# Kernel optimization log

Measured on AMD Instinct MI355X. Metric: run time of the kernel, lower is better.

Reference implementation:

```python
import jax, jax.numpy as jnp
import numpy as np

N_NODES = 50000
N_EDGES = 800000
D = 128
BATCHSIZE = 64


def setup_inputs() -> dict:
    key = jax.random.key(0)
    k1, k2, k3, k4 = jax.random.split(key, 4)
    x = jax.random.normal(k1, (N_NODES, D), dtype=jnp.float32)
    eps = jnp.zeros((1,), dtype=jnp.float32)
    W_pred = jax.random.normal(k2, (D, D), dtype=jnp.float32) * (1.0 / np.sqrt(D))
    b_pred = jnp.zeros((D,), dtype=jnp.float32)
    edge_index = jax.random.randint(k3, (2, N_EDGES), 0, N_NODES, dtype=jnp.int64)
    batch = jnp.sort(jax.random.randint(k4, (N_NODES,), 0, BATCHSIZE, dtype=jnp.int64))
    return {"x": x, "eps": eps, "W_pred": W_pred, "b_pred": b_pred,
            "edge_index": edge_index, "batch": batch}


def reference(x, eps, W_pred, b_pred, edge_index, batch):
    src, dst = edge_index[0], edge_index[1]
    # spmm: sum of neighbor features for each destination node [N, D]
    agg = jax.ops.segment_sum(x[src], dst, num_segments=N_NODES)
    # eps-weighted self update (apply_func=None, norm=None)
    out = (1.0 + eps) * x + agg
    out = jax.nn.relu(out)  # activation='relu'
    # linear_prediction then per-graph scatter-add pooling
    pooled = out @ W_pred + b_pred  # [N, pooled_features]
    pooled2 = jax.ops.segment_sum(pooled, batch, num_segments=BATCHSIZE)  # [B, pooled]
    return out, pooled2
```

## Files before the change

kernel.cpp:

```cpp
#include <hip/hip_runtime.h>
#include <hip/hip_bf16.h>

#define N_NODES 50000
#define N_EDGES 800000
#define D 128
#define BATCHSIZE 64

#define CHUNK_BITS 7
#define CHUNK 128
#define NBUCKETS 391
#define NBUCKETS_PAD 392
#define CAP 2400
#define GS_PAD 16

#define FB_TILE 2048
#define NTILES ((N_EDGES + FB_TILE - 1) / FB_TILE)
#define FB_THREADS 256
#define FB_GRID NTILES
#define EPT 8

__device__ inline unsigned f2bf(float f) {
    union { float f; unsigned u; } c; c.f = f;
    unsigned u = c.u;
    return (u + 0x7fffu + ((u >> 16) & 1u)) >> 16;
}

__device__ inline float4 bf4_to_f4(uint2 u) {
    union { unsigned u; float f; } a, b, c, d;
    a.u = u.x << 16; b.u = u.x & 0xffff0000u;
    c.u = u.y << 16; d.u = u.y & 0xffff0000u;
    float4 r; r.x = a.f; r.y = b.f; r.z = c.f; r.w = d.f;
    return r;
}

__global__ __launch_bounds__(FB_THREADS) void bin_convert_kernel(
    const float* __restrict__ x,
    unsigned short* __restrict__ xb,
    const int* __restrict__ edge_index,
    int* __restrict__ gcur,
    int* __restrict__ bucket,
    float* __restrict__ pooled2,
    int gs)
{
    __shared__ int hist[NBUCKETS_PAD];
    __shared__ int gbase[NBUCKETS_PAD];

    int t = threadIdx.x;
    int blk = blockIdx.x;

    for (int i = blk * FB_THREADS + t; i < BATCHSIZE * D; i += FB_GRID * FB_THREADS)
        pooled2[i] = 0.0f;

    if (xb != nullptr) {
        const int TOT8 = N_NODES * D / 8;
        for (int i = blk * FB_THREADS + t; i < TOT8; i += FB_GRID * FB_THREADS) {
            float4 v0 = *(const float4*)(x + (size_t)i * 8);
            float4 v1 = *(const float4*)(x + (size_t)i * 8 + 4);
            uint4 pk;
            pk.x = f2bf(v0.x) | (f2bf(v0.y) << 16);
            pk.y = f2bf(v0.z) | (f2bf(v0.w) << 16);
            pk.z = f2bf(v1.x) | (f2bf(v1.y) << 16);
            pk.w = f2bf(v1.z) | (f2bf(v1.w) << 16);
            *(uint4*)(xb + (size_t)i * 8) = pk;
        }
    }

    for (int i = t; i < NBUCKETS_PAD; i += FB_THREADS) hist[i] = 0;
    __syncthreads();

    int base = blk * FB_TILE;
    int lim = N_EDGES - base; if (lim > FB_TILE) lim = FB_TILE;

    int bkt[EPT];
    int pack[EPT];
#pragma unroll
    for (int j = 0; j < EPT / 4; ++j) {
        int e4 = (j * FB_THREADS + t) * 4;
#pragma unroll
        for (int k = 0; k < 4; ++k) bkt[j * 4 + k] = -1;
        if (e4 < lim) {
            int4 s4 = *(const int4*)(edge_index + base + e4);
            int4 d4 = *(const int4*)(edge_index + N_EDGES + base + e4);
            int ss[4] = { s4.x, s4.y, s4.z, s4.w };
            int dd[4] = { d4.x, d4.y, d4.z, d4.w };
#pragma unroll
            for (int k = 0; k < 4; ++k) {
                int b = dd[k] >> CHUNK_BITS;
                bkt[j * 4 + k] = b;
                pack[j * 4 + k] = (ss[k] << CHUNK_BITS) | (dd[k] & (CHUNK - 1));
                atomicAdd(&hist[b], 1);
            }
        }
    }
    __syncthreads();

    for (int i = t; i < NBUCKETS; i += FB_THREADS) {
        int c = hist[i];
        gbase[i] = c ? atomicAdd(&gcur[i * gs], c) : 0;
        hist[i] = 0;
    }
    __syncthreads();

#pragma unroll
    for (int k = 0; k < EPT; ++k) {
        int b = bkt[k];
        if (b >= 0) {
            int pos = gbase[b] + atomicAdd(&hist[b], 1);
            if (pos < CAP) bucket[(size_t)b * CAP + pos] = pack[k];
        }
    }
}

template<bool BF16>
__global__ __launch_bounds__(1024) void gather_kernel(
    const float* __restrict__ x,
    const unsigned short* __restrict__ xb,
    const float* __restrict__ eps,
    const int* __restrict__ batch,
    const int* __restrict__ gcur,
    const int* __restrict__ bucket,
    const float* __restrict__ W,
    const float* __restrict__ b_pred,
    float* __restrict__ out,
    float* __restrict__ pooled2,
    int gs)
{
    __shared__ int   ebuf[CAP];
    __shared__ int   sorted[CAP];
    __shared__ int   hist[CHUNK];
    __shared__ int   offs[CHUNK + 1];
    __shared__ int   cursor[CHUNK];
    __shared__ float pool[8 * D];
    __shared__ int   pcount[8];

    int c = blockIdx.x;
    int t = threadIdx.x;
    int lane = t & 31;
    int g = t >> 5;

    if (t < CHUNK) hist[t] = 0;
    if (t < 8) pcount[t] = 0;
    for (int i = t; i < 8 * D; i += 1024) pool[i] = 0.0f;
    int cnt = gcur[(size_t)c * gs];
    if (cnt > CAP) cnt = CAP;
    __syncthreads();

    for (int i = t; i < cnt; i += 1024) {
        int p = bucket[(size_t)c * CAP + i];
        ebuf[i] = p;
        atomicAdd(&hist[p & (CHUNK - 1)], 1);
    }
    __syncthreads();

    if (t < 64) {
        int h0 = hist[2 * t], h1 = hist[2 * t + 1];
        int tot = h0 + h1;
        int incl = tot;
#pragma unroll
        for (int o = 1; o < 64; o <<= 1) {
            int y = __shfl_up(incl, o, 64);
            if (t >= o) incl += y;
        }
        int excl = incl - tot;
        offs[2 * t] = excl;          cursor[2 * t] = excl;
        offs[2 * t + 1] = excl + h0; cursor[2 * t + 1] = excl + h0;
        if (t == 63) offs[CHUNK] = incl;
    }
    __syncthreads();

    for (int i = t; i < cnt; i += 1024) {
        int p = ebuf[i];
        int pos = atomicAdd(&cursor[p & (CHUNK - 1)], 1);
        sorted[pos] = p >> CHUNK_BITS;
    }
    __syncthreads();

    int node0 = c << CHUNK_BITS;
    int base_b = batch[node0];
    float scale = 1.0f + eps[0];
    int dv_cur = -1;
    float4 ps = make_float4(0.f, 0.f, 0.f, 0.f);

#pragma unroll
    for (int k = 0; k < 4; ++k) {
        int d = 4 * g + k;
        int node = node0 + d;
        if (node >= N_NODES) break;
        int start = offs[d], end = offs[d + 1];
        float4 acc = make_float4(0.f, 0.f, 0.f, 0.f);
        int i = start;
        if (BF16) {
            for (; i + 4 <= end; i += 4) {
                int s0 = sorted[i], s1 = sorted[i + 1];
                int s2 = sorted[i + 2], s3 = sorted[i + 3];
                uint2 u0 = *(const uint2*)(xb + (size_t)s0 * D + lane * 4);
                uint2 u1 = *(const uint2*)(xb + (size_t)s1 * D + lane * 4);
                uint2 u2 = *(const uint2*)(xb + (size_t)s2 * D + lane * 4);
                uint2 u3 = *(const uint2*)(xb + (size_t)s3 * D + lane * 4);
                float4 v0 = bf4_to_f4(u0), v1 = bf4_to_f4(u1);
                float4 v2 = bf4_to_f4(u2), v3 = bf4_to_f4(u3);
                acc.x += (v0.x + v1.x) + (v2.x + v3.x);
                acc.y += (v0.y + v1.y) + (v2.y + v3.y);
                acc.z += (v0.z + v1.z) + (v2.z + v3.z);
                acc.w += (v0.w + v1.w) + (v2.w + v3.w);
            }
            for (; i < end; ++i) {
                uint2 u0 = *(const uint2*)(xb + (size_t)sorted[i] * D + lane * 4);
                float4 v0 = bf4_to_f4(u0);
                acc.x += v0.x; acc.y += v0.y; acc.z += v0.z; acc.w += v0.w;
            }
        } else {
            for (; i + 4 <= end; i += 4) {
                int s0 = sorted[i], s1 = sorted[i + 1];
                int s2 = sorted[i + 2], s3 = sorted[i + 3];
                const float4 v0 = *(const float4*)(x + (size_t)s0 * D + lane * 4);
                const float4 v1 = *(const float4*)(x + (size_t)s1 * D + lane * 4);
                const float4 v2 = *(const float4*)(x + (size_t)s2 * D + lane * 4);
                const float4 v3 = *(const float4*)(x + (size_t)s3 * D + lane * 4);
                acc.x += (v0.x + v1.x) + (v2.x + v3.x);
                acc.y += (v0.y + v1.y) + (v2.y + v3.y);
                acc.z += (v0.z + v1.z) + (v2.z + v3.z);
                acc.w += (v0.w + v1.w) + (v2.w + v3.w);
            }
            for (; i < end; ++i) {
                const float4 v0 = *(const float4*)(x + (size_t)sorted[i] * D + lane * 4);
                acc.x += v0.x; acc.y += v0.y; acc.z += v0.z; acc.w += v0.w;
            }
        }
        const float4 xv = *(const float4*)(x + (size_t)node * D + lane * 4);
        float4 o;
        o.x = fmaxf(fmaf(scale, xv.x, acc.x), 0.0f);
        o.y = fmaxf(fmaf(scale, xv.y, acc.y), 0.0f);
        o.z = fmaxf(fmaf(scale, xv.z, acc.z), 0.0f);
        o.w = fmaxf(fmaf(scale, xv.w, acc.w), 0.0f);
        *(float4*)(out + (size_t)node * D + lane * 4) = o;

        int dv = batch[node] - base_b;
        if (dv < 8) {
            if (dv != dv_cur) {
                if (dv_cur >= 0) {
                    float* pp = &pool[dv_cur * D + lane * 4];
                    atomicAdd(pp + 0, ps.x); atomicAdd(pp + 1, ps.y);
                    atomicAdd(pp + 2, ps.z); atomicAdd(pp + 3, ps.w);
                }
                ps = make_float4(0.f, 0.f, 0.f, 0.f);
                dv_cur = dv;
            }
            ps.x += o.x; ps.y += o.y; ps.z += o.z; ps.w += o.w;
            if (lane == 0) atomicAdd(&pcount[dv], 1);
        }
    }
    if (dv_cur >= 0) {
        float* pp = &pool[dv_cur * D + lane * 4];
        atomicAdd(pp + 0, ps.x); atomicAdd(pp + 1, ps.y);
        atomicAdd(pp + 2, ps.z); atomicAdd(pp + 3, ps.w);
    }
    __syncthreads();

    int lastnode = node0 + CHUNK - 1;
    if (lastnode >= N_NODES) lastnode = N_NODES - 1;
    int used = batch[lastnode] - base_b + 1;
    if (used > 8) used = 8;
    if (t < D) {
        for (int dv = 0; dv < used; ++dv) {
            float acc = (float)pcount[dv] * b_pred[t];
            const float* prow = &pool[dv * D];
#pragma unroll 8
            for (int k = 0; k < D; ++k) {
                acc = fmaf(prow[k], W[(size_t)k * D + t], acc);
            }
            atomicAdd(&pooled2[(size_t)(base_b + dv) * D + t], acc);
        }
    }
}


__global__ void edge_scatter_kernel(const float* __restrict__ x,
                                    const int* __restrict__ edge_index,
                                    float* __restrict__ agg) {
    int tid = blockIdx.x * blockDim.x + threadIdx.x;
    int lane = tid & 31;
    int e = tid >> 5;
    if (e >= N_EDGES) return;
    int src = edge_index[e];
    int dst = edge_index[N_EDGES + e];
    const float4 v = *(const float4*)(x + (size_t)src * D + lane * 4);
    float* dp = agg + (size_t)dst * D + lane * 4;
    atomicAdd(dp + 0, v.x);
    atomicAdd(dp + 1, v.y);
    atomicAdd(dp + 2, v.z);
    atomicAdd(dp + 3, v.w);
}

__global__ void finalize_kernel(const float* __restrict__ x,
                                const float* __restrict__ eps,
                                const int* __restrict__ batch,
                                float* __restrict__ out,
                                float* __restrict__ Sf,
                                float* __restrict__ counts) {
    int tid = blockIdx.x * blockDim.x + threadIdx.x;
    int lane = tid & 31;
    int node = tid >> 5;
    if (node >= N_NODES) return;
    float scale = 1.0f + eps[0];
    const float4 xv = *(const float4*)(x + (size_t)node * D + lane * 4);
    float4 av = *(float4*)(out + (size_t)node * D + lane * 4);
    float4 o;
    o.x = fmaxf(fmaf(scale, xv.x, av.x), 0.0f);
    o.y = fmaxf(fmaf(scale, xv.y, av.y), 0.0f);
    o.z = fmaxf(fmaf(scale, xv.z, av.z), 0.0f);
    o.w = fmaxf(fmaf(scale, xv.w, av.w), 0.0f);
    *(float4*)(out + (size_t)node * D + lane * 4) = o;
    int b = batch[node];
    float* sp = Sf + (size_t)b * D + lane * 4;
    atomicAdd(sp + 0, o.x);
    atomicAdd(sp + 1, o.y);
    atomicAdd(sp + 2, o.z);
    atomicAdd(sp + 3, o.w);
    if (lane == 0) atomicAdd(counts + b, 1.0f);
}

__global__ void pool_gemm_fallback_kernel(const float* __restrict__ Sf,
                                          const float* __restrict__ counts,
                                          const float* __restrict__ W,
                                          const float* __restrict__ b_pred,
                                          float* __restrict__ pooled2) {
    int b = blockIdx.x;
    int j = threadIdx.x;
    float acc = counts[b] * b_pred[j];
    const float* srow = Sf + (size_t)b * D;
#pragma unroll 8
    for (int k = 0; k < D; ++k) {
        acc = fmaf(srow[k], W[(size_t)k * D + j], acc);
    }
    pooled2[(size_t)b * D + j] = acc;
}

extern "C" void kernel_launch(void* const* d_in, const int* in_sizes, int n_in,
                              void* d_out, int out_size, void* d_ws, size_t ws_size,
                              hipStream_t stream) {
    const float* x      = (const float*)d_in[0];
    const float* eps    = (const float*)d_in[1];
    const float* W_pred = (const float*)d_in[2];
    const float* b_pred = (const float*)d_in[3];
    const int*   eidx   = (const int*)d_in[4];
    const int*   batch  = (const int*)d_in[5];

    float* out     = (float*)d_out;
    float* pooled2 = (float*)d_out + (size_t)N_NODES * D;

    const size_t xb_ints = (size_t)N_NODES * D / 2;
    const size_t buck    = (size_t)NBUCKETS * CAP;

    const size_t need_pad_full  = ((size_t)NBUCKETS_PAD * GS_PAD + buck + xb_ints) * 4;
    const size_t need_full      = ((size_t)NBUCKETS_PAD + buck + xb_ints) * 4;
    const size_t need_pad_mid   = ((size_t)NBUCKETS_PAD * GS_PAD + buck) * 4;
    const size_t need_mid       = ((size_t)NBUCKETS_PAD + buck) * 4;

    if (ws_size >= need_mid) {
        int gs = (ws_size >= (ws_size >= need_full ? need_pad_full : need_pad_mid))
                     ? GS_PAD : 1;
        size_t gcur_ints = (size_t)NBUCKETS_PAD * gs;
        int* gcur   = (int*)d_ws;
        int* bucket = (int*)d_ws + gcur_ints;
        bool full = (ws_size >= (gs == GS_PAD ? need_pad_full : need_full));
        unsigned short* xb = full
            ? (unsigned short*)((int*)d_ws + gcur_ints + buck) : nullptr;

        hipMemsetAsync(gcur, 0, gcur_ints * 4, stream);

        bin_convert_kernel<<<FB_GRID, FB_THREADS, 0, stream>>>(
            x, xb, eidx, gcur, bucket, pooled2, gs);
        if (full) {
            gather_kernel<true><<<NBUCKETS, 1024, 0, stream>>>(
                x, xb, eps, batch, gcur, bucket, W_pred, b_pred, out, pooled2, gs);
        } else {
            gather_kernel<false><<<NBUCKETS, 1024, 0, stream>>>(
                x, (const unsigned short*)nullptr, eps, batch, gcur, bucket,
                W_pred, b_pred, out, pooled2, gs);
        }
    } else {
        float* Sf      = (float*)d_ws;
        float* countsf = (float*)d_ws + BATCHSIZE * D;
        hipMemsetAsync(out, 0, (size_t)N_NODES * D * sizeof(float), stream);
        hipMemsetAsync(d_ws, 0, (BATCHSIZE * D + BATCHSIZE) * sizeof(float), stream);
        {
            long long total = (long long)N_EDGES * 32;
            int blocks = (int)((total + 255) / 256);
            edge_scatter_kernel<<<blocks, 256, 0, stream>>>(x, eidx, out);
        }
        {
            long long total = (long long)N_NODES * 32;
            int blocks = (int)((total + 255) / 256);
            finalize_kernel<<<blocks, 256, 0, stream>>>(x, eps, batch, out, Sf, countsf);
        }
        pool_gemm_fallback_kernel<<<BATCHSIZE, D, 0, stream>>>(Sf, countsf, W_pred, b_pred, pooled2);
    }
}
```

Baseline: 145.8 us.

## Fuse binning and gather into one cooperative kernel with grid sync

Merges the edge-binning/bf16-conversion kernel and the per-chunk gather kernel into a single cooperative launch of 391 blocks × 512 threads, separated by a grid-wide barrier. Shared buffers are reused for the binning histogram. Each warp group now processes 8 destination nodes instead of 4. This removes a kernel launch boundary but halves per-block threads in the gather phase and adds grid-sync cost.

```diff
diff --git a/kernel.cpp b/kernel.cpp
--- a/kernel.cpp
+++ b/kernel.cpp
@@ -1,5 +1,8 @@
 #include <hip/hip_runtime.h>
 #include <hip/hip_bf16.h>
+#include <hip/hip_cooperative_groups.h>
+
+namespace cg = cooperative_groups;
 
 #define N_NODES 50000
 #define N_EDGES 800000
@@ -13,11 +16,8 @@
 #define CAP 2400
 #define GS_PAD 16
 
+#define FT 512
 #define FB_TILE 2048
-#define NTILES ((N_EDGES + FB_TILE - 1) / FB_TILE)
-#define FB_THREADS 256
-#define FB_GRID NTILES
-#define EPT 8
 
 __device__ inline unsigned f2bf(float f) {
     union { float f; unsigned u; } c; c.f = f;
@@ -33,92 +33,15 @@
     return r;
 }
 
-__global__ __launch_bounds__(FB_THREADS) void bin_convert_kernel(
+template<bool BF16>
+__global__ __launch_bounds__(FT) void fused_kernel(
     const float* __restrict__ x,
     unsigned short* __restrict__ xb,
-    const int* __restrict__ edge_index,
+    const int* __restrict__ eidx,
     int* __restrict__ gcur,
     int* __restrict__ bucket,
-    float* __restrict__ pooled2,
-    int gs)
-{
-    __shared__ int hist[NBUCKETS_PAD];
-    __shared__ int gbase[NBUCKETS_PAD];
-
-    int t = threadIdx.x;
-    int blk = blockIdx.x;
-
-    for (int i = blk * FB_THREADS + t; i < BATCHSIZE * D; i += FB_GRID * FB_THREADS)
-        pooled2[i] = 0.0f;
-
-    if (xb != nullptr) {
-        const int TOT8 = N_NODES * D / 8;
-        for (int i = blk * FB_THREADS + t; i < TOT8; i += FB_GRID * FB_THREADS) {
-            float4 v0 = *(const float4*)(x + (size_t)i * 8);
-            float4 v1 = *(const float4*)(x + (size_t)i * 8 + 4);
-            uint4 pk;
-            pk.x = f2bf(v0.x) | (f2bf(v0.y) << 16);
-            pk.y = f2bf(v0.z) | (f2bf(v0.w) << 16);
-            pk.z = f2bf(v1.x) | (f2bf(v1.y) << 16);
-            pk.w = f2bf(v1.z) | (f2bf(v1.w) << 16);
-            *(uint4*)(xb + (size_t)i * 8) = pk;
-        }
-    }
-
-    for (int i = t; i < NBUCKETS_PAD; i += FB_THREADS) hist[i] = 0;
-    __syncthreads();
-
-    int base = blk * FB_TILE;
-    int lim = N_EDGES - base; if (lim > FB_TILE) lim = FB_TILE;
-
-    int bkt[EPT];
-    int pack[EPT];
-#pragma unroll
-    for (int j = 0; j < EPT / 4; ++j) {
-        int e4 = (j * FB_THREADS + t) * 4;
-#pragma unroll
-        for (int k = 0; k < 4; ++k) bkt[j * 4 + k] = -1;
-        if (e4 < lim) {
-            int4 s4 = *(const int4*)(edge_index + base + e4);
-            int4 d4 = *(const int4*)(edge_index + N_EDGES + base + e4);
-            int ss[4] = { s4.x, s4.y, s4.z, s4.w };
-            int dd[4] = { d4.x, d4.y, d4.z, d4.w };
-#pragma unroll
-            for (int k = 0; k < 4; ++k) {
-                int b = dd[k] >> CHUNK_BITS;
-                bkt[j * 4 + k] = b;
-                pack[j * 4 + k] = (ss[k] << CHUNK_BITS) | (dd[k] & (CHUNK - 1));
-                atomicAdd(&hist[b], 1);
-            }
-        }
-    }
-    __syncthreads();
-
-    for (int i = t; i < NBUCKETS; i += FB_THREADS) {
-        int c = hist[i];
-        gbase[i] = c ? atomicAdd(&gcur[i * gs], c) : 0;
-        hist[i] = 0;
-    }
-    __syncthreads();
-
-#pragma unroll
-    for (int k = 0; k < EPT; ++k) {
-        int b = bkt[k];
-        if (b >= 0) {
-            int pos = gbase[b] + atomicAdd(&hist[b], 1);
-            if (pos < CAP) bucket[(size_t)b * CAP + pos] = pack[k];
-        }
-    }
-}
-
-template<bool BF16>
-__global__ __launch_bounds__(1024) void gather_kernel(
-    const float* __restrict__ x,
-    const unsigned short* __restrict__ xb,
     const float* __restrict__ eps,
     const int* __restrict__ batch,
-    const int* __restrict__ gcur,
-    const int* __restrict__ bucket,
     const float* __restrict__ W,
     const float* __restrict__ b_pred,
     float* __restrict__ out,
@@ -133,19 +56,88 @@
     __shared__ float pool[8 * D];
     __shared__ int   pcount[8];
 
-    int c = blockIdx.x;
     int t = threadIdx.x;
+    int blk = blockIdx.x;
+    const int GSTRIDE = NBUCKETS * FT;
+
+    int* histA  = ebuf;
+    int* gbaseA = sorted;
+
+    for (int i = blk * FT + t; i < BATCHSIZE * D; i += GSTRIDE)
+        pooled2[i] = 0.0f;
+
+    if (BF16) {
+        const int TOT8 = N_NODES * D / 8;
+        for (int i = blk * FT + t; i < TOT8; i += GSTRIDE) {
+            float4 v0 = *(const float4*)(x + (size_t)i * 8);
+            float4 v1 = *(const float4*)(x + (size_t)i * 8 + 4);
+            uint4 pk;
+            pk.x = f2bf(v0.x) | (f2bf(v0.y) << 16);
+            pk.y = f2bf(v0.z) | (f2bf(v0.w) << 16);
+            pk.z = f2bf(v1.x) | (f2bf(v1.y) << 16);
+            pk.w = f2bf(v1.z) | (f2bf(v1.w) << 16);
+            *(uint4*)(xb + (size_t)i * 8) = pk;
+        }
+    }
+
+    for (int i = t; i < NBUCKETS_PAD; i += FT) histA[i] = 0;
+    __syncthreads();
+
+    int base = blk * FB_TILE;
+    int lim = N_EDGES - base; if (lim > FB_TILE) lim = FB_TILE;
+
+    int bkt[4];
+    int pack[4];
+    {
+        int e4 = t * 4;
+#pragma unroll
+        for (int k = 0; k < 4; ++k) bkt[k] = -1;
+        if (e4 < lim) {
+            int4 s4 = *(const int4*)(eidx + base + e4);
+            int4 d4 = *(const int4*)(eidx + N_EDGES + base + e4);
+            int ss[4] = { s4.x, s4.y, s4.z, s4.w };
+            int dd[4] = { d4.x, d4.y, d4.z, d4.w };
+#pragma unroll
+            for (int k = 0; k < 4; ++k) {
+                int b = dd[k] >> CHUNK_BITS;
+                bkt[k] = b;
+                pack[k] = (ss[k] << CHUNK_BITS) | (dd[k] & (CHUNK - 1));
+                atomicAdd(&histA[b], 1);
+            }
+        }
+    }
+    __syncthreads();
+
+    for (int i = t; i < NBUCKETS; i += FT) {
+        int cc = histA[i];
+        gbaseA[i] = cc ? atomicAdd(&gcur[(size_t)i * gs], cc) : 0;
+        histA[i] = 0;
+    }
+    __syncthreads();
+
+#pragma unroll
+    for (int k = 0; k < 4; ++k) {
+        int b = bkt[k];
+        if (b >= 0) {
+            int pos = gbaseA[b] + atomicAdd(&histA[b], 1);
+            if (pos < CAP) bucket[(size_t)b * CAP + pos] = pack[k];
+        }
+    }
+
+    cg::this_grid().sync();
+
+    int c = blk;
     int lane = t & 31;
     int g = t >> 5;
 
     if (t < CHUNK) hist[t] = 0;
     if (t < 8) pcount[t] = 0;
-    for (int i = t; i < 8 * D; i += 1024) pool[i] = 0.0f;
+    for (int i = t; i < 8 * D; i += FT) pool[i] = 0.0f;
     int cnt = gcur[(size_t)c * gs];
     if (cnt > CAP) cnt = CAP;
     __syncthreads();
 
-    for (int i = t; i < cnt; i += 1024) {
+    for (int i = t; i < cnt; i += FT) {
         int p = bucket[(size_t)c * CAP + i];
         ebuf[i] = p;
         atomicAdd(&hist[p & (CHUNK - 1)], 1);
@@ -168,7 +160,7 @@
     }
     __syncthreads();
 
-    for (int i = t; i < cnt; i += 1024) {
+    for (int i = t; i < cnt; i += FT) {
         int p = ebuf[i];
         int pos = atomicAdd(&cursor[p & (CHUNK - 1)], 1);
         sorted[pos] = p >> CHUNK_BITS;
@@ -182,8 +174,8 @@
     float4 ps = make_float4(0.f, 0.f, 0.f, 0.f);
 
 #pragma unroll
-    for (int k = 0; k < 4; ++k) {
-        int d = 4 * g + k;
+    for (int k = 0; k < 8; ++k) {
+        int d = 8 * g + k;
         int node = node0 + d;
         if (node >= N_NODES) break;
         int start = offs[d], end = offs[d + 1];
@@ -369,15 +361,23 @@
 
         hipMemsetAsync(gcur, 0, gcur_ints * 4, stream);
 
-        bin_convert_kernel<<<FB_GRID, FB_THREADS, 0, stream>>>(
-            x, xb, eidx, gcur, bucket, pooled2, gs);
         if (full) {
-            gather_kernel<true><<<NBUCKETS, 1024, 0, stream>>>(
-                x, xb, eps, batch, gcur, bucket, W_pred, b_pred, out, pooled2, gs);
+            auto kfun = fused_kernel<true>;
+            void* args[] = { (void*)&x, (void*)&xb, (void*)&eidx, (void*)&gcur,
+                             (void*)&bucket, (void*)&eps, (void*)&batch,
+                             (void*)&W_pred, (void*)&b_pred, (void*)&out,
+                             (void*)&pooled2, (void*)&gs };
+            hipLaunchCooperativeKernel(reinterpret_cast<void*>(kfun),
+                                       dim3(NBUCKETS), dim3(FT), args, 0, stream);
         } else {
-            gather_kernel<false><<<NBUCKETS, 1024, 0, stream>>>(
-                x, (const unsigned short*)nullptr, eps, batch, gcur, bucket,
-                W_pred, b_pred, out, pooled2, gs);
+            unsigned short* xb_null = nullptr;
+            auto kfun = fused_kernel<false>;
+            void* args[] = { (void*)&x, (void*)&xb_null, (void*)&eidx, (void*)&gcur,
+                             (void*)&bucket, (void*)&eps, (void*)&batch,
+                             (void*)&W_pred, (void*)&b_pred, (void*)&out,
+                             (void*)&pooled2, (void*)&gs };
+            hipLaunchCooperativeKernel(reinterpret_cast<void*>(kfun),
+                                       dim3(NBUCKETS), dim3(FT), args, 0, stream);
         }
     } else {
         float* Sf      = (float*)d_ws;
```

Measured after the change: 231.5 us. 58.8% more time.

## Slice gather by source-node range so all warps sweep x in lockstep

Applied to the files above, without the earlier changes.

Sorts each chunk's edges by (source slice, destination) with a 512-bin histogram and shared-memory scan. The gather loop then runs over four source-node slices, keeping per-node accumulators in registers, so all warps in a block touch the same region of x at the same time for better L2/cache locality. Launch bounds are also raised to request two blocks per CU. In exchange it adds a multi-barrier Hillis-Steele scan, more shared memory and more registers, and each warp's work is split into more, shorter loops.

```diff
diff --git a/kernel.cpp b/kernel.cpp
--- a/kernel.cpp
+++ b/kernel.cpp
@@ -12,6 +12,10 @@
 #define NBUCKETS_PAD 392
 #define CAP 2400
 #define GS_PAD 16
+
+#define NSLICE 4
+#define SLICE_DIV 12500
+#define NBINS (NSLICE * CHUNK)
 
 #define FB_TILE 2048
 #define NTILES ((N_EDGES + FB_TILE - 1) / FB_TILE)
@@ -112,7 +116,7 @@
 }
 
 template<bool BF16>
-__global__ __launch_bounds__(1024) void gather_kernel(
+__global__ __launch_bounds__(1024, 2) void gather_kernel(
     const float* __restrict__ x,
     const unsigned short* __restrict__ xb,
     const float* __restrict__ eps,
@@ -127,9 +131,9 @@
 {
     __shared__ int   ebuf[CAP];
     __shared__ int   sorted[CAP];
-    __shared__ int   hist[CHUNK];
-    __shared__ int   offs[CHUNK + 1];
-    __shared__ int   cursor[CHUNK];
+    __shared__ int   hist[NBINS];
+    __shared__ int   offs[NBINS + 1];
+    __shared__ int   cursor[NBINS];
     __shared__ float pool[8 * D];
     __shared__ int   pcount[8];
 
@@ -138,7 +142,7 @@
     int lane = t & 31;
     int g = t >> 5;
 
-    if (t < CHUNK) hist[t] = 0;
+    for (int i = t; i < NBINS; i += 1024) hist[i] = 0;
     if (t < 8) pcount[t] = 0;
     for (int i = t; i < 8 * D; i += 1024) pool[i] = 0.0f;
     int cnt = gcur[(size_t)c * gs];
@@ -148,29 +152,30 @@
     for (int i = t; i < cnt; i += 1024) {
         int p = bucket[(size_t)c * CAP + i];
         ebuf[i] = p;
-        atomicAdd(&hist[p & (CHUNK - 1)], 1);
-    }
-    __syncthreads();
-
-    if (t < 64) {
-        int h0 = hist[2 * t], h1 = hist[2 * t + 1];
-        int tot = h0 + h1;
-        int incl = tot;
-#pragma unroll
-        for (int o = 1; o < 64; o <<= 1) {
-            int y = __shfl_up(incl, o, 64);
-            if (t >= o) incl += y;
-        }
-        int excl = incl - tot;
-        offs[2 * t] = excl;          cursor[2 * t] = excl;
-        offs[2 * t + 1] = excl + h0; cursor[2 * t + 1] = excl + h0;
-        if (t == 63) offs[CHUNK] = incl;
-    }
+        int key = (int)((unsigned)(p >> CHUNK_BITS) / SLICE_DIV) * CHUNK + (p & (CHUNK - 1));
+        atomicAdd(&hist[key], 1);
+    }
+    __syncthreads();
+
+    if (t < NBINS) cursor[t] = hist[t];
+    __syncthreads();
+    for (int st = 1; st < NBINS; st <<= 1) {
+        int v = 0;
+        if (t < NBINS && t >= st) v = cursor[t - st];
+        __syncthreads();
+        if (t < NBINS) cursor[t] += v;
+        __syncthreads();
+    }
+    if (t < NBINS) offs[t + 1] = cursor[t];
+    if (t == 0) offs[0] = 0;
+    __syncthreads();
+    if (t < NBINS) cursor[t] = offs[t];
     __syncthreads();
 
     for (int i = t; i < cnt; i += 1024) {
         int p = ebuf[i];
-        int pos = atomicAdd(&cursor[p & (CHUNK - 1)], 1);
+        int key = (int)((unsigned)(p >> CHUNK_BITS) / SLICE_DIV) * CHUNK + (p & (CHUNK - 1));
+        int pos = atomicAdd(&cursor[key], 1);
         sorted[pos] = p >> CHUNK_BITS;
     }
     __syncthreads();
@@ -178,61 +183,71 @@
     int node0 = c << CHUNK_BITS;
     int base_b = batch[node0];
     float scale = 1.0f + eps[0];
+
+    float4 acc[4];
+#pragma unroll
+    for (int k = 0; k < 4; ++k) acc[k] = make_float4(0.f, 0.f, 0.f, 0.f);
+
+    for (int s = 0; s < NSLICE; ++s) {
+#pragma unroll
+        for (int k = 0; k < 4; ++k) {
+            int d = 4 * g + k;
+            int i = offs[s * CHUNK + d], end = offs[s * CHUNK + d + 1];
+            float4 a = acc[k];
+            if (BF16) {
+                for (; i + 4 <= end; i += 4) {
+                    int s0 = sorted[i], s1 = sorted[i + 1];
+                    int s2 = sorted[i + 2], s3 = sorted[i + 3];
+                    uint2 u0 = *(const uint2*)(xb + (size_t)s0 * D + lane * 4);
+                    uint2 u1 = *(const uint2*)(xb + (size_t)s1 * D + lane * 4);
+                    uint2 u2 = *(const uint2*)(xb + (size_t)s2 * D + lane * 4);
+                    uint2 u3 = *(const uint2*)(xb + (size_t)s3 * D + lane * 4);
+                    float4 v0 = bf4_to_f4(u0), v1 = bf4_to_f4(u1);
+                    float4 v2 = bf4_to_f4(u2), v3 = bf4_to_f4(u3);
+                    a.x += (v0.x + v1.x) + (v2.x + v3.x);
+                    a.y += (v0.y + v1.y) + (v2.y + v3.y);
+                    a.z += (v0.z + v1.z) + (v2.z + v3.z);
+                    a.w += (v0.w + v1.w) + (v2.w + v3.w);
+                }
+                for (; i < end; ++i) {
+                    uint2 u0 = *(const uint2*)(xb + (size_t)sorted[i] * D + lane * 4);
+                    float4 v0 = bf4_to_f4(u0);
+                    a.x += v0.x; a.y += v0.y; a.z += v0.z; a.w += v0.w;
+                }
+            } else {
+                for (; i + 4 <= end; i += 4) {
+                    int s0 = sorted[i], s1 = sorted[i + 1];
+                    int s2 = sorted[i + 2], s3 = sorted[i + 3];
+                    const float4 v0 = *(const float4*)(x + (size_t)s0 * D + lane * 4);
+                    const float4 v1 = *(const float4*)(x + (size_t)s1 * D + lane * 4);
+                    const float4 v2 = *(const float4*)(x + (size_t)s2 * D + lane * 4);
+                    const float4 v3 = *(const float4*)(x + (size_t)s3 * D + lane * 4);
+                    a.x += (v0.x + v1.x) + (v2.x + v3.x);
+                    a.y += (v0.y + v1.y) + (v2.y + v3.y);
+                    a.z += (v0.z + v1.z) + (v2.z + v3.z);
+                    a.w += (v0.w + v1.w) + (v2.w + v3.w);
+                }
+                for (; i < end; ++i) {
+                    const float4 v0 = *(const float4*)(x + (size_t)sorted[i] * D + lane * 4);
+                    a.x += v0.x; a.y += v0.y; a.z += v0.z; a.w += v0.w;
+                }
+            }
+            acc[k] = a;
+        }
+    }
+
     int dv_cur = -1;
     float4 ps = make_float4(0.f, 0.f, 0.f, 0.f);
-
 #pragma unroll
     for (int k = 0; k < 4; ++k) {
-        int d = 4 * g + k;
-        int node = node0 + d;
+        int node = node0 + 4 * g + k;
         if (node >= N_NODES) break;
-        int start = offs[d], end = offs[d + 1];
-        float4 acc = make_float4(0.f, 0.f, 0.f, 0.f);
-        int i = start;
-        if (BF16) {
-            for (; i + 4 <= end; i += 4) {
-                int s0 = sorted[i], s1 = sorted[i + 1];
-                int s2 = sorted[i + 2], s3 = sorted[i + 3];
-                uint2 u0 = *(const uint2*)(xb + (size_t)s0 * D + lane * 4);
-                uint2 u1 = *(const uint2*)(xb + (size_t)s1 * D + lane * 4);
-                uint2 u2 = *(const uint2*)(xb + (size_t)s2 * D + lane * 4);
-                uint2 u3 = *(const uint2*)(xb + (size_t)s3 * D + lane * 4);
-                float4 v0 = bf4_to_f4(u0), v1 = bf4_to_f4(u1);
-                float4 v2 = bf4_to_f4(u2), v3 = bf4_to_f4(u3);
-                acc.x += (v0.x + v1.x) + (v2.x + v3.x);
-                acc.y += (v0.y + v1.y) + (v2.y + v3.y);
-                acc.z += (v0.z + v1.z) + (v2.z + v3.z);
-                acc.w += (v0.w + v1.w) + (v2.w + v3.w);
-            }
-            for (; i < end; ++i) {
-                uint2 u0 = *(const uint2*)(xb + (size_t)sorted[i] * D + lane * 4);
-                float4 v0 = bf4_to_f4(u0);
-                acc.x += v0.x; acc.y += v0.y; acc.z += v0.z; acc.w += v0.w;
-            }
-        } else {
-            for (; i + 4 <= end; i += 4) {
-                int s0 = sorted[i], s1 = sorted[i + 1];
-                int s2 = sorted[i + 2], s3 = sorted[i + 3];
-                const float4 v0 = *(const float4*)(x + (size_t)s0 * D + lane * 4);
-                const float4 v1 = *(const float4*)(x + (size_t)s1 * D + lane * 4);
-                const float4 v2 = *(const float4*)(x + (size_t)s2 * D + lane * 4);
-                const float4 v3 = *(const float4*)(x + (size_t)s3 * D + lane * 4);
-                acc.x += (v0.x + v1.x) + (v2.x + v3.x);
-                acc.y += (v0.y + v1.y) + (v2.y + v3.y);
-                acc.z += (v0.z + v1.z) + (v2.z + v3.z);
-                acc.w += (v0.w + v1.w) + (v2.w + v3.w);
-            }
-            for (; i < end; ++i) {
-                const float4 v0 = *(const float4*)(x + (size_t)sorted[i] * D + lane * 4);
-                acc.x += v0.x; acc.y += v0.y; acc.z += v0.z; acc.w += v0.w;
-            }
-        }
         const float4 xv = *(const float4*)(x + (size_t)node * D + lane * 4);
         float4 o;
-        o.x = fmaxf(fmaf(scale, xv.x, acc.x), 0.0f);
-        o.y = fmaxf(fmaf(scale, xv.y, acc.y), 0.0f);
-        o.z = fmaxf(fmaf(scale, xv.z, acc.z), 0.0f);
-        o.w = fmaxf(fmaf(scale, xv.w, acc.w), 0.0f);
+        o.x = fmaxf(fmaf(scale, xv.x, acc[k].x), 0.0f);
+        o.y = fmaxf(fmaf(scale, xv.y, acc[k].y), 0.0f);
+        o.z = fmaxf(fmaf(scale, xv.z, acc[k].z), 0.0f);
+        o.w = fmaxf(fmaf(scale, xv.w, acc[k].w), 0.0f);
         *(float4*)(out + (size_t)node * D + lane * 4) = o;
 
         int dv = batch[node] - base_b;
@@ -263,13 +278,13 @@
     if (used > 8) used = 8;
     if (t < D) {
         for (int dv = 0; dv < used; ++dv) {
-            float acc = (float)pcount[dv] * b_pred[t];
+            float acc2 = (float)pcount[dv] * b_pred[t];
             const float* prow = &pool[dv * D];
 #pragma unroll 8
             for (int k = 0; k < D; ++k) {
-                acc = fmaf(prow[k], W[(size_t)k * D + t], acc);
+                acc2 = fmaf(prow[k], W[(size_t)k * D + t], acc2);
             }
-            atomicAdd(&pooled2[(size_t)(base_b + dv) * D + t], acc);
+            atomicAdd(&pooled2[(size_t)(base_b + dv) * D + t], acc2);
         }
     }
 }
```

Measured after the change: 145.7 us, median of 2. Within noise of the previous version (-0.1%).

## Replace chunk bucketing and in-block sort with per-node fixed-capacity adjacency slots

Applied to the files above, without the earlier changes.

Edge binning now writes each source index straight into a fixed per-destination slot array (48 slots per node) using a global atomic counter per node. This removes the per-chunk bucket histogram, prefix scan and shared-memory counting sort in the gather kernel, which now just loads its 128 nodes' slot lists into shared memory. The cost is 800k scattered global atomics on 50k counters in place of block-local atomics, and silent truncation of any node with more than 48 in-edges. Launch bounds now request two 1024-thread blocks per CU.

```diff
diff --git a/kernel.cpp b/kernel.cpp
--- a/kernel.cpp
+++ b/kernel.cpp
@@ -9,15 +9,11 @@
 #define CHUNK_BITS 7
 #define CHUNK 128
 #define NBUCKETS 391
-#define NBUCKETS_PAD 392
-#define CAP 2400
-#define GS_PAD 16
-
-#define FB_TILE 2048
-#define NTILES ((N_EDGES + FB_TILE - 1) / FB_TILE)
+#define NNODE_PAD 50048
+#define SEG_CAP 48
+
 #define FB_THREADS 256
-#define FB_GRID NTILES
-#define EPT 8
+#define FB_GRID 391
 
 __device__ inline unsigned f2bf(float f) {
     union { float f; unsigned u; } c; c.f = f;
@@ -33,27 +29,25 @@
     return r;
 }
 
-__global__ __launch_bounds__(FB_THREADS) void bin_convert_kernel(
+__global__ __launch_bounds__(FB_THREADS) void csr_bin_convert(
     const float* __restrict__ x,
     unsigned short* __restrict__ xb,
     const int* __restrict__ edge_index,
-    int* __restrict__ gcur,
-    int* __restrict__ bucket,
-    float* __restrict__ pooled2,
-    int gs)
+    int* __restrict__ cnt,
+    int* __restrict__ seg,
+    float* __restrict__ pooled2)
 {
-    __shared__ int hist[NBUCKETS_PAD];
-    __shared__ int gbase[NBUCKETS_PAD];
-
     int t = threadIdx.x;
     int blk = blockIdx.x;
-
-    for (int i = blk * FB_THREADS + t; i < BATCHSIZE * D; i += FB_GRID * FB_THREADS)
+    int gid = blk * FB_THREADS + t;
+    const int gsz = FB_GRID * FB_THREADS;
+
+    for (int i = gid; i < BATCHSIZE * D; i += gsz)
         pooled2[i] = 0.0f;
 
     if (xb != nullptr) {
         const int TOT8 = N_NODES * D / 8;
-        for (int i = blk * FB_THREADS + t; i < TOT8; i += FB_GRID * FB_THREADS) {
+        for (int i = gid; i < TOT8; i += gsz) {
             float4 v0 = *(const float4*)(x + (size_t)i * 8);
             float4 v1 = *(const float4*)(x + (size_t)i * 8 + 4);
             uint4 pk;
@@ -65,71 +59,35 @@
         }
     }
 
-    for (int i = t; i < NBUCKETS_PAD; i += FB_THREADS) hist[i] = 0;
-    __syncthreads();
-
-    int base = blk * FB_TILE;
-    int lim = N_EDGES - base; if (lim > FB_TILE) lim = FB_TILE;
-
-    int bkt[EPT];
-    int pack[EPT];
+    const int TOTE4 = N_EDGES / 4;
+    for (int q = gid; q < TOTE4; q += gsz) {
+        int4 s4 = ((const int4*)edge_index)[q];
+        int4 d4 = ((const int4*)(edge_index + N_EDGES))[q];
+        int ss[4] = { s4.x, s4.y, s4.z, s4.w };
+        int dd[4] = { d4.x, d4.y, d4.z, d4.w };
 #pragma unroll
-    for (int j = 0; j < EPT / 4; ++j) {
-        int e4 = (j * FB_THREADS + t) * 4;
-#pragma unroll
-        for (int k = 0; k < 4; ++k) bkt[j * 4 + k] = -1;
-        if (e4 < lim) {
-            int4 s4 = *(const int4*)(edge_index + base + e4);
-            int4 d4 = *(const int4*)(edge_index + N_EDGES + base + e4);
-            int ss[4] = { s4.x, s4.y, s4.z, s4.w };
-            int dd[4] = { d4.x, d4.y, d4.z, d4.w };
-#pragma unroll
-            for (int k = 0; k < 4; ++k) {
-                int b = dd[k] >> CHUNK_BITS;
-                bkt[j * 4 + k] = b;
-                pack[j * 4 + k] = (ss[k] << CHUNK_BITS) | (dd[k] & (CHUNK - 1));
-                atomicAdd(&hist[b], 1);
-            }
-        }
-    }
-    __syncthreads();
-
-    for (int i = t; i < NBUCKETS; i += FB_THREADS) {
-        int c = hist[i];
-        gbase[i] = c ? atomicAdd(&gcur[i * gs], c) : 0;
-        hist[i] = 0;
-    }
-    __syncthreads();
-
-#pragma unroll
-    for (int k = 0; k < EPT; ++k) {
-        int b = bkt[k];
-        if (b >= 0) {
-            int pos = gbase[b] + atomicAdd(&hist[b], 1);
-            if (pos < CAP) bucket[(size_t)b * CAP + pos] = pack[k];
+        for (int k = 0; k < 4; ++k) {
+            int pos = atomicAdd(&cnt[dd[k]], 1);
+            if (pos < SEG_CAP) seg[(size_t)dd[k] * SEG_CAP + pos] = ss[k];
         }
     }
 }
 
 template<bool BF16>
-__global__ __launch_bounds__(1024) void gather_kernel(
+__global__ __launch_bounds__(1024, 2) void gather_csr(
     const float* __restrict__ x,
     const unsigned short* __restrict__ xb,
     const float* __restrict__ eps,
     const int* __restrict__ batch,
-    const int* __restrict__ gcur,
-    const int* __restrict__ bucket,
+    const int* __restrict__ cnt,
+    const int* __restrict__ seg,
     const float* __restrict__ W,
     const float* __restrict__ b_pred,
     float* __restrict__ out,
-    float* __restrict__ pooled2,
-    int gs)
+    float* __restrict__ pooled2)
 {
-    __shared__ int   ebuf[CAP];
-    __shared__ int   sorted[CAP];
-    __shared__ int   hist[CHUNK];
-    __shared__ int   offs[CHUNK + 1];
-    __shared__ int   cursor[CHUNK];
+    __shared__ int   segL[CHUNK * SEG_CAP];
+    __shared__ int   cntL[CHUNK];
     __shared__ float pool[8 * D];
     __shared__ int   pcount[8];
 
@@ -137,46 +95,23 @@
     int t = threadIdx.x;
     int lane = t & 31;
     int g = t >> 5;
-
-    if (t < CHUNK) hist[t] = 0;
+    int node0 = c << CHUNK_BITS;
+
+    if (t < CHUNK) {
+        int n = node0 + t;
+        int cc = (n < N_NODES) ? cnt[n] : 0;
+        cntL[t] = cc > SEG_CAP ? SEG_CAP : cc;
+    }
     if (t < 8) pcount[t] = 0;
     for (int i = t; i < 8 * D; i += 1024) pool[i] = 0.0f;
-    int cnt = gcur[(size_t)c * gs];
-    if (cnt > CAP) cnt = CAP;
+
+    for (int i = t; i < CHUNK * SEG_CAP; i += 1024) {
+        int n = node0 + i / SEG_CAP;
+        segL[i] = (n < N_NODES) ? seg[(size_t)node0 * SEG_CAP + i] : 0;
+    }
     __syncthreads();
 
-    for (int i = t; i < cnt; i += 1024) {
-        int p = bucket[(size_t)c * CAP + i];
-        ebuf[i] = p;
-        atomicAdd(&hist[p & (CHUNK - 1)], 1);
-    }
-    __syncthreads();
-
-    if (t < 64) {
-        int h0 = hist[2 * t], h1 = hist[2 * t + 1];
-        int tot = h0 + h1;
-        int incl = tot;
-#pragma unroll
-        for (int o = 1; o < 64; o <<= 1) {
-            int y = __shfl_up(incl, o, 64);
-            if (t >= o) incl += y;
-        }
-        int excl = incl - tot;
-        offs[2 * t] = excl;          cursor[2 * t] = excl;
-        offs[2 * t + 1] = excl + h0; cursor[2 * t + 1] = excl + h0;
-        if (t == 63) offs[CHUNK] = incl;
-    }
-    __syncthreads();
-
-    for (int i = t; i < cnt; i += 1024) {
-        int p = ebuf[i];
-        int pos = atomicAdd(&cursor[p & (CHUNK - 1)], 1);
-        sorted[pos] = p >> CHUNK_BITS;
-    }
-    __syncthreads();
-
-    int node0 = c << CHUNK_BITS;
-    int base_b = batch[node0];
+    int base_b = batch[node0 < N_NODES ? node0 : N_NODES - 1];
     float scale = 1.0f + eps[0];
     int dv_cur = -1;
     float4 ps = make_float4(0.f, 0.f, 0.f, 0.f);
@@ -186,13 +121,14 @@
         int d = 4 * g + k;
         int node = node0 + d;
         if (node >= N_NODES) break;
-        int start = offs[d], end = offs[d + 1];
+        const int* sp = &segL[d * SEG_CAP];
+        int end = cntL[d];
         float4 acc = make_float4(0.f, 0.f, 0.f, 0.f);
-        int i = start;
+        int i = 0;
         if (BF16) {
             for (; i + 4 <= end; i += 4) {
-                int s0 = sorted[i], s1 = sorted[i + 1];
-                int s2 = sorted[i + 2], s3 = sorted[i + 3];
+                int s0 = sp[i], s1 = sp[i + 1];
+                int s2 = sp[i + 2], s3 = sp[i + 3];
                 uint2 u0 = *(const uint2*)(xb + (size_t)s0 * D + lane * 4);
                 uint2 u1 = *(const uint2*)(xb + (size_t)s1 * D + lane * 4);
                 uint2 u2 = *(const uint2*)(xb + (size_t)s2 * D + lane * 4);
@@ -205,14 +141,14 @@
                 acc.w += (v0.w + v1.w) + (v2.w + v3.w);
             }
             for (; i < end; ++i) {
-                uint2 u0 = *(const uint2*)(xb + (size_t)sorted[i] * D + lane * 4);
+                uint2 u0 = *(const uint2*)(xb + (size_t)sp[i] * D + lane * 4);
                 float4 v0 = bf4_to_f4(u0);
                 acc.x += v0.x; acc.y += v0.y; acc.z += v0.z; acc.w += v0.w;
             }
         } else {
             for (; i + 4 <= end; i += 4) {
-                int s0 = sorted[i], s1 = sorted[i + 1];
-                int s2 = sorted[i + 2], s3 = sorted[i + 3];
+                int s0 = sp[i], s1 = sp[i + 1];
+                int s2 = sp[i + 2], s3 = sp[i + 3];
                 const float4 v0 = *(const float4*)(x + (size_t)s0 * D + lane * 4);
                 const float4 v1 = *(const float4*)(x + (size_t)s1 * D + lane * 4);
                 const float4 v2 = *(const float4*)(x + (size_t)s2 * D + lane * 4);
@@ -223,7 +159,7 @@
                 acc.w += (v0.w + v1.w) + (v2.w + v3.w);
             }
             for (; i < end; ++i) {
-                const float4 v0 = *(const float4*)(x + (size_t)sorted[i] * D + lane * 4);
+                const float4 v0 = *(const float4*)(x + (size_t)sp[i] * D + lane * 4);
                 acc.x += v0.x; acc.y += v0.y; acc.z += v0.z; acc.w += v0.w;
             }
         }
@@ -263,13 +199,13 @@
     if (used > 8) used = 8;
     if (t < D) {
         for (int dv = 0; dv < used; ++dv) {
-            float acc = (float)pcount[dv] * b_pred[t];
+            float acc2 = (float)pcount[dv] * b_pred[t];
             const float* prow = &pool[dv * D];
 #pragma unroll 8
             for (int k = 0; k < D; ++k) {
-                acc = fmaf(prow[k], W[(size_t)k * D + t], acc);
-            }
-            atomicAdd(&pooled2[(size_t)(base_b + dv) * D + t], acc);
+                acc2 = fmaf(prow[k], W[(size_t)k * D + t], acc2);
+            }
+            atomicAdd(&pooled2[(size_t)(base_b + dv) * D + t], acc2);
         }
     }
 }
@@ -349,35 +285,29 @@
     float* out     = (float*)d_out;
     float* pooled2 = (float*)d_out + (size_t)N_NODES * D;
 
-    const size_t xb_ints = (size_t)N_NODES * D / 2;
-    const size_t buck    = (size_t)NBUCKETS * CAP;
-
-    const size_t need_pad_full  = ((size_t)NBUCKETS_PAD * GS_PAD + buck + xb_ints) * 4;
-    const size_t need_full      = ((size_t)NBUCKETS_PAD + buck + xb_ints) * 4;
-    const size_t need_pad_mid   = ((size_t)NBUCKETS_PAD * GS_PAD + buck) * 4;
-    const size_t need_mid       = ((size_t)NBUCKETS_PAD + buck) * 4;
-
-    if (ws_size >= need_mid) {
-        int gs = (ws_size >= (ws_size >= need_full ? need_pad_full : need_pad_mid))
-                     ? GS_PAD : 1;
-        size_t gcur_ints = (size_t)NBUCKETS_PAD * gs;
-        int* gcur   = (int*)d_ws;
-        int* bucket = (int*)d_ws + gcur_ints;
-        bool full = (ws_size >= (gs == GS_PAD ? need_pad_full : need_full));
+    const size_t xb_ints  = (size_t)N_NODES * D / 2;
+    const size_t csr_ints = (size_t)NNODE_PAD * (1 + SEG_CAP);
+    const size_t need_csr_full = (csr_ints + xb_ints) * 4;
+    const size_t need_csr_mid  = csr_ints * 4;
+
+    if (ws_size >= need_csr_mid) {
+        int* cnt = (int*)d_ws;
+        int* seg = cnt + NNODE_PAD;
+        bool full = (ws_size >= need_csr_full);
         unsigned short* xb = full
-            ? (unsigned short*)((int*)d_ws + gcur_ints + buck) : nullptr;
-
-        hipMemsetAsync(gcur, 0, gcur_ints * 4, stream);
-
-        bin_convert_kernel<<<FB_GRID, FB_THREADS, 0, stream>>>(
-            x, xb, eidx, gcur, bucket, pooled2, gs);
+            ? (unsigned short*)(seg + (size_t)NNODE_PAD * SEG_CAP) : nullptr;
+
+        hipMemsetAsync(cnt, 0, (size_t)NNODE_PAD * 4, stream);
+
+        csr_bin_convert<<<FB_GRID, FB_THREADS, 0, stream>>>(
+            x, xb, eidx, cnt, seg, pooled2);
         if (full) {
-            gather_kernel<true><<<NBUCKETS, 1024, 0, stream>>>(
-                x, xb, eps, batch, gcur, bucket, W_pred, b_pred, out, pooled2, gs);
+            gather_csr<true><<<NBUCKETS, 1024, 0, stream>>>(
+                x, xb, eps, batch, cnt, seg, W_pred, b_pred, out, pooled2);
         } else {
-            gather_kernel<false><<<NBUCKETS, 1024, 0, stream>>>(
-                x, (const unsigned short*)nullptr, eps, batch, gcur, bucket,
-                W_pred, b_pred, out, pooled2, gs);
+            gather_csr<false><<<NBUCKETS, 1024, 0, stream>>>(
+                x, (const unsigned short*)nullptr, eps, batch, cnt, seg,
+                W_pred, b_pred, out, pooled2);
         }
     } else {
         float* Sf      = (float*)d_ws;
```

Measured after the change: 177.8 us. 1.22x slower.
